# Performance work log

Measured on AMD Instinct MI355X. Metric: run time of the kernel, lower is better.

## Reference

```python
import jax, jax.numpy as jnp
import numpy as np

N_NODES = 100000
N_EDGES = 3200000
NFEAT, NHID, NCLASS = 512, 256, 40


def setup_inputs() -> dict:
    key = jax.random.key(0)
    ks = jax.random.split(key, 8)
    x = jax.random.normal(ks[0], (N_NODES, NFEAT), dtype=jnp.float32)
    edge_row = jax.random.randint(ks[1], (N_EDGES,), 0, N_NODES, dtype=jnp.int32)
    edge_col = jax.random.randint(ks[2], (N_EDGES,), 0, N_NODES, dtype=jnp.int32)
    edge_val = jax.random.uniform(ks[3], (N_EDGES,), dtype=jnp.float32)
    W1 = jax.random.normal(ks[4], (NFEAT, NHID), dtype=jnp.float32) * (1.0 / np.sqrt(NFEAT))
    b1 = jnp.zeros((NHID,), dtype=jnp.float32)
    W2 = jax.random.normal(ks[5], (NHID, NCLASS), dtype=jnp.float32) * (1.0 / np.sqrt(NHID))
    b2 = jnp.zeros((NCLASS,), dtype=jnp.float32)
    return {"x": x, "edge_row": edge_row, "edge_col": edge_col, "edge_val": edge_val,
            "W1": W1, "b1": b1, "W2": W2, "b2": b2}


def _spmm(edge_row, edge_col, edge_val, dense):
    # out[i] = sum_{e: row[e]==i} val[e] * dense[col[e]]
    gathered = dense[edge_col] * edge_val[:, None]
    return jax.ops.segment_sum(gathered, edge_row, num_segments=N_NODES)


def reference(x, edge_row, edge_col, edge_val, W1, b1, W2, b2):
    # GraphConvolution 1: support = x@W1; out = adj @ support + b1; relu
    h = _spmm(edge_row, edge_col, edge_val, x @ W1) + b1
    h = jax.nn.relu(h)
    # dropout: inference mode (training=False) -> identity
    # GraphConvolution 2
    logits = _spmm(edge_row, edge_col, edge_val, h @ W2) + b2
    return jax.nn.log_softmax(logits, axis=1)
```

## Files before the change

kernel.cpp:

```cpp
#include <hip/hip_runtime.h>
#include <hip/hip_bf16.h>
#include <math.h>

#define N_NODES 100000
#define N_EDGES 3200000
#define NFEAT 512
#define NHID 256
#define NCLASS 40
#define LDP 40
#define NB1 256
#define RPB1 391
#define NBLK 256
#define CHUNK 12500

#if __has_builtin(__builtin_amdgcn_cvt_pk_fp8_f32) && __has_builtin(__builtin_amdgcn_cvt_pk_f32_fp8)
#define SUP_FP8 1
#else
#define SUP_FP8 0
#endif

typedef short bf16x8 __attribute__((ext_vector_type(8)));
typedef float f32x4 __attribute__((ext_vector_type(4)));
typedef float f32x2 __attribute__((ext_vector_type(2)));
typedef unsigned long long u64;

__device__ __forceinline__ unsigned short f2bf(float f) {
    unsigned int u = __builtin_bit_cast(unsigned int, f);
    u += 0x7fffu + ((u >> 16) & 1u);
    return (unsigned short)(u >> 16);
}
__device__ __forceinline__ float bflo(unsigned int u) { return __builtin_bit_cast(float, u << 16); }
__device__ __forceinline__ float bfhi(unsigned int u) { return __builtin_bit_cast(float, u & 0xffff0000u); }
__device__ __forceinline__ unsigned int ecol_of(u64 ev) { return (unsigned int)(ev & 0xffffffffu); }
__device__ __forceinline__ float eval_of(u64 ev) { return __builtin_bit_cast(float, (unsigned int)(ev >> 32)); }

__global__ __launch_bounds__(256) void k_histA(const int* __restrict__ erow, int* __restrict__ hist) {
    __shared__ int lh[NB1];
    const int t = threadIdx.x, blk = blockIdx.x;
    lh[t] = 0;
    __syncthreads();
    const int base = blk * CHUNK;
    for (int i = t; i < CHUNK; i += 256)
        atomicAdd(&lh[erow[base + i] / RPB1], 1);
    __syncthreads();
    hist[blk * NB1 + t] = lh[t];
}

__global__ __launch_bounds__(256) void k_scanB(const int* __restrict__ hist,
                                               int* __restrict__ offs, int* __restrict__ bucketptr) {
    __shared__ int sd[256];
    const int b = threadIdx.x;
    int run = 0;
#pragma unroll 8
    for (int blk = 0; blk < NBLK; ++blk) {
        int v = hist[blk * NB1 + b];
        offs[blk * NB1 + b] = run;
        run += v;
    }
    sd[b] = run;
    __syncthreads();
    for (int off = 1; off < 256; off <<= 1) {
        int x = (b >= off) ? sd[b - off] : 0;
        __syncthreads();
        sd[b] += x;
        __syncthreads();
    }
    bucketptr[b] = sd[b] - run;
    if (b == 255) bucketptr[NB1] = sd[255];
}

__global__ __launch_bounds__(256) void k_scatC(const int* __restrict__ erow, const int* __restrict__ ecol,
                                               const float* __restrict__ eval_,
                                               const int* __restrict__ offs, const int* __restrict__ bucketptr,
                                               u64* __restrict__ tmp) {
    __shared__ u64 srec[CHUNK];
    __shared__ unsigned char sbkt[CHUNK];
    __shared__ int lcnt[NB1];
    __shared__ int lscan[NB1];
    __shared__ int lcur[NB1];
    __shared__ int lsegbase[NB1];
    const int t = threadIdx.x, blk = blockIdx.x;
    const int base = blk * CHUNK;
    lcnt[t] = 0;
    lsegbase[t] = bucketptr[t] + offs[blk * NB1 + t];
    __syncthreads();
    for (int i = t; i < CHUNK; i += 256)
        atomicAdd(&lcnt[erow[base + i] / RPB1], 1);
    __syncthreads();
    {
        __shared__ int sd[256];
        int v = lcnt[t];
        sd[t] = v;
        __syncthreads();
        for (int off = 1; off < 256; off <<= 1) {
            int x = (t >= off) ? sd[t - off] : 0;
            __syncthreads();
            sd[t] += x;
            __syncthreads();
        }
        lscan[t] = sd[t] - v;
        lcur[t] = sd[t] - v;
    }
    __syncthreads();
    for (int i = t; i < CHUNK; i += 256) {
        int r = erow[base + i];
        int c = ecol[base + i];
        unsigned int vb = __builtin_bit_cast(unsigned int, eval_[base + i]);
        int b = r / RPB1;
        int rl = r - b * RPB1;
        int pos = atomicAdd(&lcur[b], 1);
        srec[pos] = (u64)((unsigned int)c | ((unsigned int)rl << 17)) | ((u64)vb << 32);
        sbkt[pos] = (unsigned char)b;
    }
    __syncthreads();
    for (int i = t; i < CHUNK; i += 256) {
        int b = sbkt[i];
        tmp[lsegbase[b] + (i - lscan[b])] = srec[i];
    }
}

__global__ __launch_bounds__(512) void k_sortD(const int* __restrict__ bucketptr, const u64* __restrict__ tmp,
                                               u64* __restrict__ pedge, int* __restrict__ rowptr) {
    __shared__ int lcnt[512];
    __shared__ int sc[512];
    __shared__ int lcur[512];
    const int b = blockIdx.x, t = threadIdx.x;
    const int beg = bucketptr[b], end = bucketptr[b + 1];
    const int n = end - beg;
    lcnt[t] = 0;
    __syncthreads();
    for (int i = t; i < n; i += 512)
        atomicAdd(&lcnt[(int)((tmp[beg + i] >> 17) & 0x1ff)], 1);
    __syncthreads();
    sc[t] = lcnt[t];
    __syncthreads();
    for (int off = 1; off < 512; off <<= 1) {
        int x = (t >= off) ? sc[t - off] : 0;
        __syncthreads();
        sc[t] += x;
        __syncthreads();
    }
    int excl = sc[t] - lcnt[t];
    lcur[t] = excl;
    if (t < RPB1) {
        int row = b * RPB1 + t;
        if (row < N_NODES) rowptr[row] = beg + excl;
    }
    if (b == NB1 - 1 && t == 0) rowptr[N_NODES] = N_EDGES;
    __syncthreads();
    for (int i = t; i < n; i += 512) {
        u64 rec = tmp[beg + i];
        int rl = (int)((rec >> 17) & 0x1ff);
        int pos = atomicAdd(&lcur[rl], 1);
        pedge[beg + pos] = rec & 0xFFFFFFFF0001FFFFull;
    }
}

__global__ void k_wt(const float* __restrict__ W1, const float* __restrict__ W2,
                     unsigned short* __restrict__ W1T, unsigned short* __restrict__ W2T) {
    int i = blockIdx.x * 256 + threadIdx.x;
    int nn = i >> 9, k = i & 511;
    W1T[i] = f2bf(W1[k * NHID + nn]);
    if (i < 64 * NHID) {
        int n2 = i >> 8, k2 = i & 255;
        W2T[i] = (n2 < NCLASS) ? f2bf(W2[k2 * NCLASS + n2]) : (unsigned short)0;
    }
}

__global__ __launch_bounds__(512) void k_gemm1(const float* __restrict__ X,
                                               const unsigned short* __restrict__ W1T,
                                               unsigned char* __restrict__ support8) {
    __shared__ unsigned short As[128 * LDP];
    __shared__ unsigned short Bs[256 * LDP];
    const int t = threadIdx.x;
    const int lane = t & 63;
    const int w = t >> 6;
    const int wm = w >> 2, wn = w & 3;
    const int l15 = lane & 15, l4 = lane >> 4;
    const int bm = blockIdx.x;

    f32x4 acc[4][4];
#pragma unroll
    for (int m = 0; m < 4; ++m)
#pragma unroll
        for (int n = 0; n < 4; ++n) acc[m][n] = (f32x4){0.f, 0.f, 0.f, 0.f};

    const int arow = t >> 2, aq = t & 3;
    const long growA = (long)bm * 128 + arow;
    const bool avalid = growA < N_NODES;
    const float* xsrc = X + growA * NFEAT + aq * 8;
    unsigned short* adst = &As[arow * LDP + aq * 8];
    const int brow = t >> 1, bhalf = t & 1;
    const unsigned short* bsrc = W1T + (long)brow * NFEAT + bhalf * 16;
    unsigned short* bdst = &Bs[brow * LDP + bhalf * 16];

    for (int kt = 0; kt < NFEAT; kt += 32) {
        union { float4 v4[2]; float f[8]; } a;
        if (avalid) {
            a.v4[0] = *(const float4*)(xsrc + kt + 0);
            a.v4[1] = *(const float4*)(xsrc + kt + 4);
        } else {
            a.v4[0] = make_float4(0.f, 0.f, 0.f, 0.f);
            a.v4[1] = make_float4(0.f, 0.f, 0.f, 0.f);
        }
        union { uint4 q; unsigned short us[8]; } u;
#pragma unroll
        for (int j = 0; j < 8; ++j) u.us[j] = f2bf(a.f[j]);
        uint4 b0 = *(const uint4*)(bsrc + kt);
        uint4 b1v = *(const uint4*)(bsrc + kt + 8);
        *(uint4*)(adst) = u.q;
        *(uint4*)(bdst) = b0;
        *(uint4*)(bdst + 8) = b1v;
        __syncthreads();

        bf16x8 afr[4], bfr[4];
#pragma unroll
        for (int m = 0; m < 4; ++m)
            afr[m] = *(const bf16x8*)&As[(wm * 64 + m * 16 + l15) * LDP + l4 * 8];
#pragma unroll
        for (int n = 0; n < 4; ++n)
            bfr[n] = *(const bf16x8*)&Bs[(wn * 64 + n * 16 + l15) * LDP + l4 * 8];
#pragma unroll
        for (int m = 0; m < 4; ++m)
#pragma unroll
            for (int n = 0; n < 4; ++n)
                acc[m][n] = __builtin_amdgcn_mfma_f32_16x16x32_bf16(bfr[n], afr[m], acc[m][n], 0, 0, 0);
        __syncthreads();
    }
#pragma unroll
    for (int m = 0; m < 4; ++m) {
        long row = (long)bm * 128 + wm * 64 + m * 16 + l15;
        if (row < N_NODES) {
#pragma unroll
            for (int n = 0; n < 4; ++n) {
                int colb = wn * 64 + n * 16 + l4 * 4;
#if SUP_FP8
                int wv = 0;
                wv = __builtin_amdgcn_cvt_pk_fp8_f32(acc[m][n][0], acc[m][n][1], wv, false);
                wv = __builtin_amdgcn_cvt_pk_fp8_f32(acc[m][n][2], acc[m][n][3], wv, true);
                *(unsigned int*)&support8[(size_t)row * NHID + colb] = (unsigned int)wv;
#else
                ushort4 o;
                o.x = f2bf(acc[m][n][0]);
                o.y = f2bf(acc[m][n][1]);
                o.z = f2bf(acc[m][n][2]);
                o.w = f2bf(acc[m][n][3]);
                *(ushort4*)&support8[(size_t)row * NHID * 2 + colb * 2] = o;
#endif
            }
        }
    }
}

__global__ __launch_bounds__(256) void k_spmm1(const int* __restrict__ rowptr,
                                               const u64* __restrict__ pedge,
                                               const unsigned char* __restrict__ support8,
                                               const float* __restrict__ b1,
                                               unsigned short* __restrict__ h) {
    int wrow = (blockIdx.x * 256 + threadIdx.x) >> 6;
    int lane = threadIdx.x & 63;
    if (wrow >= N_NODES) return;
    int beg = rowptr[wrow], end = rowptr[wrow + 1];
    float a0 = 0.f, a1 = 0.f, a2 = 0.f, a3 = 0.f;
    const int c4 = lane * 4;
    int e = beg;
#if SUP_FP8
    for (; e + 8 <= end; e += 8) {
        u64 ev[8];
#pragma unroll
        for (int j = 0; j < 8; ++j) ev[j] = __builtin_nontemporal_load(&pedge[e + j]);
        unsigned int g[8];
#pragma unroll
        for (int j = 0; j < 8; ++j)
            g[j] = *(const unsigned int*)&support8[(size_t)ecol_of(ev[j]) * NHID + c4];
#pragma unroll
        for (int j = 0; j < 8; ++j) {
            float v = eval_of(ev[j]);
            f32x2 lo = __builtin_amdgcn_cvt_pk_f32_fp8(g[j], false);
            f32x2 hi = __builtin_amdgcn_cvt_pk_f32_fp8(g[j], true);
            a0 = fmaf(v, lo[0], a0); a1 = fmaf(v, lo[1], a1);
            a2 = fmaf(v, hi[0], a2); a3 = fmaf(v, hi[1], a3);
        }
    }
    for (; e < end; ++e) {
        u64 ev = __builtin_nontemporal_load(&pedge[e]);
        float v = eval_of(ev);
        unsigned int g = *(const unsigned int*)&support8[(size_t)ecol_of(ev) * NHID + c4];
        f32x2 lo = __builtin_amdgcn_cvt_pk_f32_fp8(g, false);
        f32x2 hi = __builtin_amdgcn_cvt_pk_f32_fp8(g, true);
        a0 = fmaf(v, lo[0], a0); a1 = fmaf(v, lo[1], a1);
        a2 = fmaf(v, hi[0], a2); a3 = fmaf(v, hi[1], a3);
    }
#else
    for (; e + 8 <= end; e += 8) {
        u64 ev[8];
#pragma unroll
        for (int j = 0; j < 8; ++j) ev[j] = __builtin_nontemporal_load(&pedge[e + j]);
        uint2 g[8];
#pragma unroll
        for (int j = 0; j < 8; ++j)
            g[j] = *(const uint2*)&support8[((size_t)ecol_of(ev[j]) * NHID + c4) * 2];
#pragma unroll
        for (int j = 0; j < 8; ++j) {
            float v = eval_of(ev[j]);
            a0 = fmaf(v, bflo(g[j].x), a0); a1 = fmaf(v, bfhi(g[j].x), a1);
            a2 = fmaf(v, bflo(g[j].y), a2); a3 = fmaf(v, bfhi(g[j].y), a3);
        }
    }
    for (; e < end; ++e) {
        u64 ev = __builtin_nontemporal_load(&pedge[e]);
        float v = eval_of(ev);
        uint2 g = *(const uint2*)&support8[((size_t)ecol_of(ev) * NHID + c4) * 2];
        a0 = fmaf(v, bflo(g.x), a0); a1 = fmaf(v, bfhi(g.x), a1);
        a2 = fmaf(v, bflo(g.y), a2); a3 = fmaf(v, bfhi(g.y), a3);
    }
#endif
    float4 bb = *(const float4*)&b1[c4];
    a0 = fmaxf(a0 + bb.x, 0.f);
    a1 = fmaxf(a1 + bb.y, 0.f);
    a2 = fmaxf(a2 + bb.z, 0.f);
    a3 = fmaxf(a3 + bb.w, 0.f);
    ushort4 o;
    o.x = f2bf(a0); o.y = f2bf(a1); o.z = f2bf(a2); o.w = f2bf(a3);
    *(ushort4*)&h[(size_t)wrow * NHID + c4] = o;
}

__global__ __launch_bounds__(256) void k_gemm2(const unsigned short* __restrict__ H,
                                               const unsigned short* __restrict__ W2T,
                                               unsigned short* __restrict__ logits2b) {
    __shared__ unsigned short As[128 * LDP];
    __shared__ unsigned short Bs[64 * LDP];
    const int t = threadIdx.x;
    const int lane = t & 63;
    const int w = t >> 6;
    const int wm = w >> 1, wn = w & 1;
    const int l15 = lane & 15, l4 = lane >> 4;
    const int bm = blockIdx.x;

    f32x4 acc[4][2];
#pragma unroll
    for (int m = 0; m < 4; ++m)
#pragma unroll
        for (int n = 0; n < 2; ++n) acc[m][n] = (f32x4){0.f, 0.f, 0.f, 0.f};

    const int srow = t >> 1, shalf = t & 1;
    const long grow = (long)bm * 128 + srow;
    const bool avalid = grow < N_NODES;
    const unsigned short* asrc = H + grow * NHID + shalf * 16;
    const int bn2 = t >> 2, bq = t & 3;
    const unsigned short* bsrc = W2T + bn2 * NHID + bq * 8;

    for (int kt = 0; kt < NHID; kt += 32) {
        uint4 a0, a1;
        if (avalid) {
            a0 = *(const uint4*)(asrc + kt);
            a1 = *(const uint4*)(asrc + kt + 8);
        } else {
            a0 = make_uint4(0, 0, 0, 0);
            a1 = make_uint4(0, 0, 0, 0);
        }
        uint4 bv = *(const uint4*)(bsrc + kt);
        *(uint4*)&As[srow * LDP + shalf * 16] = a0;
        *(uint4*)&As[srow * LDP + shalf * 16 + 8] = a1;
        *(uint4*)&Bs[bn2 * LDP + bq * 8] = bv;
        __syncthreads();

        bf16x8 afr[4], bfr[2];
#pragma unroll
        for (int m = 0; m < 4; ++m)
            afr[m] = *(const bf16x8*)&As[(wm * 64 + m * 16 + l15) * LDP + l4 * 8];
#pragma unroll
        for (int n = 0; n < 2; ++n)
            bfr[n] = *(const bf16x8*)&Bs[(wn * 32 + n * 16 + l15) * LDP + l4 * 8];
#pragma unroll
        for (int m = 0; m < 4; ++m)
#pragma unroll
            for (int n = 0; n < 2; ++n)
                acc[m][n] = __builtin_amdgcn_mfma_f32_16x16x32_bf16(bfr[n], afr[m], acc[m][n], 0, 0, 0);
        __syncthreads();
    }
#pragma unroll
    for (int m = 0; m < 4; ++m) {
        long row = (long)bm * 128 + wm * 64 + m * 16 + l15;
        if (row < N_NODES) {
#pragma unroll
            for (int n = 0; n < 2; ++n) {
                int colb = wn * 32 + n * 16 + l4 * 4;
                if (colb < NCLASS) {
                    ushort4 o;
                    o.x = f2bf(acc[m][n][0]);
                    o.y = f2bf(acc[m][n][1]);
                    o.z = f2bf(acc[m][n][2]);
                    o.w = f2bf(acc[m][n][3]);
                    *(ushort4*)&logits2b[(size_t)row * NCLASS + colb] = o;
                }
            }
        }
    }
}

__global__ __launch_bounds__(256) void k_spmm2(const int* __restrict__ rowptr,
                                               const u64* __restrict__ pedge,
                                               const unsigned short* __restrict__ logits2b,
                                               const float* __restrict__ b2, float* __restrict__ out) {
    int wrow = (blockIdx.x * 256 + threadIdx.x) >> 6;
    int lane = threadIdx.x & 63;
    if (wrow >= N_NODES) return;
    int beg = rowptr[wrow], end = rowptr[wrow + 1];
    bool act = lane < 20;
    int cp = act ? lane * 2 : 0;
    float a0 = 0.f, a1 = 0.f;
    int e = beg;
    for (; e + 8 <= end; e += 8) {
        u64 ev[8];
#pragma unroll
        for (int j = 0; j < 8; ++j) ev[j] = __builtin_nontemporal_load(&pedge[e + j]);
        unsigned int g[8];
#pragma unroll
        for (int j = 0; j < 8; ++j)
            g[j] = *(const unsigned int*)&logits2b[(size_t)ecol_of(ev[j]) * NCLASS + cp];
#pragma unroll
        for (int j = 0; j < 8; ++j) {
            float v = eval_of(ev[j]);
            a0 = fmaf(v, bflo(g[j]), a0);
            a1 = fmaf(v, bfhi(g[j]), a1);
        }
    }
    for (; e < end; ++e) {
        u64 ev = __builtin_nontemporal_load(&pedge[e]);
        float v = eval_of(ev);
        unsigned int g = *(const unsigned int*)&logits2b[(size_t)ecol_of(ev) * NCLASS + cp];
        a0 = fmaf(v, bflo(g), a0);
        a1 = fmaf(v, bfhi(g), a1);
    }
    float2 bb = *(const float2*)&b2[cp];
    a0 += bb.x;
    a1 += bb.y;
    float mv = act ? fmaxf(a0, a1) : -INFINITY;
#pragma unroll
    for (int off = 32; off; off >>= 1) mv = fmaxf(mv, __shfl_xor(mv, off, 64));
    float s = act ? (__expf(a0 - mv) + __expf(a1 - mv)) : 0.f;
#pragma unroll
    for (int off = 32; off; off >>= 1) s += __shfl_xor(s, off, 64);
    if (act) {
        float ls = __logf(s);
        float2 o;
        o.x = a0 - mv - ls;
        o.y = a1 - mv - ls;
        *(float2*)&out[(size_t)wrow * NCLASS + cp] = o;
    }
}

extern "C" void kernel_launch(void* const* d_in, const int* in_sizes, int n_in,
                              void* d_out, int out_size, void* d_ws, size_t ws_size,
                              hipStream_t stream) {
    const float* x    = (const float*)d_in[0];
    const int*   erow = (const int*)d_in[1];
    const int*   ecol = (const int*)d_in[2];
    const float* eval_ = (const float*)d_in[3];
    const float* W1   = (const float*)d_in[4];
    const float* b1   = (const float*)d_in[5];
    const float* W2   = (const float*)d_in[6];
    const float* b2   = (const float*)d_in[7];
    float* out = (float*)d_out;

    char* p = (char*)d_ws;
    auto alloc = [&](size_t b) { char* r = p; p += (b + 255) & ~(size_t)255; return r; };
    int* hist              = (int*)alloc((size_t)NBLK * NB1 * 4);
    int* offs              = (int*)alloc((size_t)NBLK * NB1 * 4);
    int* bucketptr         = (int*)alloc((size_t)(NB1 + 1) * 4);
    int* rowptr            = (int*)alloc((size_t)(N_NODES + 1) * 4);
    u64* tmp               = (u64*)alloc((size_t)N_EDGES * 8);
    u64* pedge             = (u64*)alloc((size_t)N_EDGES * 8);
    unsigned short* W1T    = (unsigned short*)alloc((size_t)NHID * NFEAT * 2);
    unsigned short* W2T    = (unsigned short*)alloc((size_t)64 * NHID * 2);
    unsigned char* support8= (unsigned char*)alloc((size_t)N_NODES * NHID * 2);
    unsigned short* h      = (unsigned short*)alloc((size_t)N_NODES * NHID * 2);
    unsigned short* logits2b = (unsigned short*)alloc((size_t)N_NODES * NCLASS * 2);

    k_histA<<<NBLK, 256, 0, stream>>>(erow, hist);
    k_scanB<<<1, 256, 0, stream>>>(hist, offs, bucketptr);
    k_scatC<<<NBLK, 256, 0, stream>>>(erow, ecol, eval_, offs, bucketptr, tmp);
    k_sortD<<<NB1, 512, 0, stream>>>(bucketptr, tmp, pedge, rowptr);
    k_wt<<<(NHID * NFEAT) / 256, 256, 0, stream>>>(W1, W2, W1T, W2T);
    k_gemm1<<<(N_NODES + 127) / 128, 512, 0, stream>>>(x, W1T, support8);
    k_spmm1<<<(N_NODES + 3) / 4, 256, 0, stream>>>(rowptr, pedge, support8, b1, h);
    k_gemm2<<<(N_NODES + 127) / 128, 256, 0, stream>>>(h, W2T, logits2b);
    k_spmm2<<<(N_NODES + 3) / 4, 256, 0, stream>>>(rowptr, pedge, logits2b, b2, out);
}
```

Measured before the change: 471.4 us.

## Double-buffer GEMM1 LDS tiles, reuse histogram in scatter, cache bucket in LDS

The first GEMM now uses two LDS buffers and prefetches the next K-tile into registers while the MFMAs run on the current tile. This halves the barriers and hides global load latency. The scatter kernel reuses the per-block histogram already computed by k_histA instead of recounting rows with shared atomics. The bucket sort kernel caches up to SCAP records in LDS so the second pass avoids re-reading global memory. The cost is more LDS use, which may lower occupancy, and buckets larger than SCAP still fall back to global reads for the overflow.

```diff
diff --git a/kernel.cpp b/kernel.cpp
--- a/kernel.cpp
+++ b/kernel.cpp
@@ -12,6 +12,7 @@
 #define RPB1 391
 #define NBLK 256
 #define CHUNK 12500
+#define SCAP 13312
 
 #if __has_builtin(__builtin_amdgcn_cvt_pk_fp8_f32) && __has_builtin(__builtin_amdgcn_cvt_pk_f32_fp8)
 #define SUP_FP8 1
@@ -71,36 +72,29 @@
 
 __global__ __launch_bounds__(256) void k_scatC(const int* __restrict__ erow, const int* __restrict__ ecol,
                                                const float* __restrict__ eval_,
+                                               const int* __restrict__ hist,
                                                const int* __restrict__ offs, const int* __restrict__ bucketptr,
                                                u64* __restrict__ tmp) {
     __shared__ u64 srec[CHUNK];
     __shared__ unsigned char sbkt[CHUNK];
-    __shared__ int lcnt[NB1];
     __shared__ int lscan[NB1];
     __shared__ int lcur[NB1];
     __shared__ int lsegbase[NB1];
+    __shared__ int sd[256];
     const int t = threadIdx.x, blk = blockIdx.x;
     const int base = blk * CHUNK;
-    lcnt[t] = 0;
     lsegbase[t] = bucketptr[t] + offs[blk * NB1 + t];
-    __syncthreads();
-    for (int i = t; i < CHUNK; i += 256)
-        atomicAdd(&lcnt[erow[base + i] / RPB1], 1);
-    __syncthreads();
-    {
-        __shared__ int sd[256];
-        int v = lcnt[t];
-        sd[t] = v;
-        __syncthreads();
-        for (int off = 1; off < 256; off <<= 1) {
-            int x = (t >= off) ? sd[t - off] : 0;
-            __syncthreads();
-            sd[t] += x;
-            __syncthreads();
-        }
-        lscan[t] = sd[t] - v;
-        lcur[t] = sd[t] - v;
-    }
+    int v = hist[blk * NB1 + t];
+    sd[t] = v;
+    __syncthreads();
+    for (int off = 1; off < 256; off <<= 1) {
+        int x = (t >= off) ? sd[t - off] : 0;
+        __syncthreads();
+        sd[t] += x;
+        __syncthreads();
+    }
+    lscan[t] = sd[t] - v;
+    lcur[t] = sd[t] - v;
     __syncthreads();
     for (int i = t; i < CHUNK; i += 256) {
         int r = erow[base + i];
@@ -121,6 +115,7 @@
 
 __global__ __launch_bounds__(512) void k_sortD(const int* __restrict__ bucketptr, const u64* __restrict__ tmp,
                                                u64* __restrict__ pedge, int* __restrict__ rowptr) {
+    __shared__ u64 srec[SCAP];
     __shared__ int lcnt[512];
     __shared__ int sc[512];
     __shared__ int lcur[512];
@@ -129,8 +124,11 @@
     const int n = end - beg;
     lcnt[t] = 0;
     __syncthreads();
-    for (int i = t; i < n; i += 512)
-        atomicAdd(&lcnt[(int)((tmp[beg + i] >> 17) & 0x1ff)], 1);
+    for (int i = t; i < n; i += 512) {
+        u64 rec = tmp[beg + i];
+        if (i < SCAP) srec[i] = rec;
+        atomicAdd(&lcnt[(int)((rec >> 17) & 0x1ff)], 1);
+    }
     __syncthreads();
     sc[t] = lcnt[t];
     __syncthreads();
@@ -149,7 +147,7 @@
     if (b == NB1 - 1 && t == 0) rowptr[N_NODES] = N_EDGES;
     __syncthreads();
     for (int i = t; i < n; i += 512) {
-        u64 rec = tmp[beg + i];
+        u64 rec = (i < SCAP) ? srec[i] : tmp[beg + i];
         int rl = (int)((rec >> 17) & 0x1ff);
         int pos = atomicAdd(&lcur[rl], 1);
         pedge[beg + pos] = rec & 0xFFFFFFFF0001FFFFull;
@@ -170,8 +168,8 @@
 __global__ __launch_bounds__(512) void k_gemm1(const float* __restrict__ X,
                                                const unsigned short* __restrict__ W1T,
                                                unsigned char* __restrict__ support8) {
-    __shared__ unsigned short As[128 * LDP];
-    __shared__ unsigned short Bs[256 * LDP];
+    __shared__ unsigned short As[2][128 * LDP];
+    __shared__ unsigned short Bs[2][256 * LDP];
     const int t = threadIdx.x;
     const int lane = t & 63;
     const int w = t >> 6;
@@ -189,44 +187,76 @@
     const long growA = (long)bm * 128 + arow;
     const bool avalid = growA < N_NODES;
     const float* xsrc = X + growA * NFEAT + aq * 8;
-    unsigned short* adst = &As[arow * LDP + aq * 8];
     const int brow = t >> 1, bhalf = t & 1;
     const unsigned short* bsrc = W1T + (long)brow * NFEAT + bhalf * 16;
-    unsigned short* bdst = &Bs[brow * LDP + bhalf * 16];
-
-    for (int kt = 0; kt < NFEAT; kt += 32) {
-        union { float4 v4[2]; float f[8]; } a;
-        if (avalid) {
-            a.v4[0] = *(const float4*)(xsrc + kt + 0);
-            a.v4[1] = *(const float4*)(xsrc + kt + 4);
-        } else {
-            a.v4[0] = make_float4(0.f, 0.f, 0.f, 0.f);
-            a.v4[1] = make_float4(0.f, 0.f, 0.f, 0.f);
-        }
+    const int adoff = arow * LDP + aq * 8;
+    const int bdoff = brow * LDP + bhalf * 16;
+
+    float4 a0r, a1r;
+    uint4 b0r, b1r;
+    if (avalid) {
+        a0r = *(const float4*)(xsrc + 0);
+        a1r = *(const float4*)(xsrc + 4);
+    } else {
+        a0r = make_float4(0.f, 0.f, 0.f, 0.f);
+        a1r = make_float4(0.f, 0.f, 0.f, 0.f);
+    }
+    b0r = *(const uint4*)(bsrc + 0);
+    b1r = *(const uint4*)(bsrc + 8);
+    {
         union { uint4 q; unsigned short us[8]; } u;
-#pragma unroll
-        for (int j = 0; j < 8; ++j) u.us[j] = f2bf(a.f[j]);
-        uint4 b0 = *(const uint4*)(bsrc + kt);
-        uint4 b1v = *(const uint4*)(bsrc + kt + 8);
-        *(uint4*)(adst) = u.q;
-        *(uint4*)(bdst) = b0;
-        *(uint4*)(bdst + 8) = b1v;
-        __syncthreads();
+        const float* af = (const float*)&a0r;
+#pragma unroll
+        for (int j = 0; j < 4; ++j) u.us[j] = f2bf(af[j]);
+        const float* af1 = (const float*)&a1r;
+#pragma unroll
+        for (int j = 0; j < 4; ++j) u.us[4 + j] = f2bf(af1[j]);
+        *(uint4*)&As[0][adoff] = u.q;
+        *(uint4*)&Bs[0][bdoff] = b0r;
+        *(uint4*)&Bs[0][bdoff + 8] = b1r;
+    }
+    __syncthreads();
+
+    for (int ki = 0; ki < 16; ++ki) {
+        const int cur = ki & 1;
+        if (ki < 15) {
+            int kt = (ki + 1) * 32;
+            if (avalid) {
+                a0r = *(const float4*)(xsrc + kt);
+                a1r = *(const float4*)(xsrc + kt + 4);
+            }
+            b0r = *(const uint4*)(bsrc + kt);
+            b1r = *(const uint4*)(bsrc + kt + 8);
+        }
 
         bf16x8 afr[4], bfr[4];
 #pragma unroll
         for (int m = 0; m < 4; ++m)
-            afr[m] = *(const bf16x8*)&As[(wm * 64 + m * 16 + l15) * LDP + l4 * 8];
+            afr[m] = *(const bf16x8*)&As[cur][(wm * 64 + m * 16 + l15) * LDP + l4 * 8];
 #pragma unroll
         for (int n = 0; n < 4; ++n)
-            bfr[n] = *(const bf16x8*)&Bs[(wn * 64 + n * 16 + l15) * LDP + l4 * 8];
+            bfr[n] = *(const bf16x8*)&Bs[cur][(wn * 64 + n * 16 + l15) * LDP + l4 * 8];
 #pragma unroll
         for (int m = 0; m < 4; ++m)
 #pragma unroll
             for (int n = 0; n < 4; ++n)
                 acc[m][n] = __builtin_amdgcn_mfma_f32_16x16x32_bf16(bfr[n], afr[m], acc[m][n], 0, 0, 0);
-        __syncthreads();
-    }
+
+        if (ki < 15) {
+            union { uint4 q; unsigned short us[8]; } u;
+            const float* af = (const float*)&a0r;
+#pragma unroll
+            for (int j = 0; j < 4; ++j) u.us[j] = avalid ? f2bf(af[j]) : (unsigned short)0;
+            const float* af1 = (const float*)&a1r;
+#pragma unroll
+            for (int j = 0; j < 4; ++j) u.us[4 + j] = avalid ? f2bf(af1[j]) : (unsigned short)0;
+            *(uint4*)&As[cur ^ 1][adoff] = u.q;
+            *(uint4*)&Bs[cur ^ 1][bdoff] = b0r;
+            *(uint4*)&Bs[cur ^ 1][bdoff + 8] = b1r;
+        }
+        __syncthreads();
+    }
+
 #pragma unroll
     for (int m = 0; m < 4; ++m) {
         long row = (long)bm * 128 + wm * 64 + m * 16 + l15;
@@ -480,7 +510,7 @@
 
     k_histA<<<NBLK, 256, 0, stream>>>(erow, hist);
     k_scanB<<<1, 256, 0, stream>>>(hist, offs, bucketptr);
-    k_scatC<<<NBLK, 256, 0, stream>>>(erow, ecol, eval_, offs, bucketptr, tmp);
+    k_scatC<<<NBLK, 256, 0, stream>>>(erow, ecol, eval_, hist, offs, bucketptr, tmp);
     k_sortD<<<NB1, 512, 0, stream>>>(bucketptr, tmp, pedge, rowptr);
     k_wt<<<(NHID * NFEAT) / 256, 256, 0, stream>>>(W1, W2, W1T, W2T);
     k_gemm1<<<(N_NODES + 127) / 128, 512, 0, stream>>>(x, W1T, support8);
```

New measurement: 458.8 us. -2.7%, faster.
